# Performance work log

Hardware: AMD Instinct MI355X
Metric: run time of the kernel (lower is better)

Reference implementation:

```python
import jax, jax.numpy as jnp
import numpy as np

# Production-scale dims (see shape_source)
B, H, W, C = 8, 64, 64, 256
KH, KW = 3, 3
BASES = 16
FILTERS = 256


def setup_inputs() -> dict:
    key = jax.random.key(0)
    k1, k2, k3, k4 = jax.random.split(key, 4)
    x = jax.random.normal(k1, (B, H, W, C), dtype=jnp.float32)
    # P: channel-mixing matrix [C, C] (initialized to identity in build, then assigned)
    P = jax.random.normal(k2, (C, C), dtype=jnp.float32) * 0.05
    # Q: per-channel basis kernels [C, kh, kw, bases]
    Q = jax.random.normal(k3, (C, KH, KW, BASES), dtype=jnp.float32) * 0.1
    # S: basis-combination weights [C, bases, filters]
    S = jax.random.normal(k4, (C, BASES, FILTERS), dtype=jnp.float32) * 0.05
    return {"x": x, "P": P, "Q": Q, "S": S}


def reference(x, P, Q, S):
    # --- Step 1: channel mixing (the vectorized_map over calculate_J) ---
    # J[o] = sum_c x[..., c] * P[o, c]  ->  one GEMM over channels
    mixed = jnp.einsum('bhwc,oc->bhwo', x, P)  # [B,H,W,C]

    C_ = P.shape[0]
    kh, kw, bases = Q.shape[1], Q.shape[2], Q.shape[3]

    # --- Step 2: per-channel conv with `bases` basis kernels (the map_fn loop) ---
    # Expressed as ONE grouped (depthwise-style) conv: group c produces outputs
    # [c*bases : (c+1)*bases], matching kernel flatten order (c, b).
    rhs = jnp.transpose(Q, (1, 2, 0, 3)).reshape(kh, kw, 1, C_ * bases)  # HWIO
    dw = jax.lax.conv_general_dilated(
        mixed, rhs, window_strides=(1, 1), padding='VALID',
        dimension_numbers=('NHWC', 'HWIO', 'NHWC'),
        feature_group_count=C_,
    )  # [B, H-kh+1, W-kw+1, C*bases], channel index k = c*bases + b

    b, h, w, _ = dw.shape
    # tau in the original: [B, h, w, bases, C]
    tau = dw.reshape(b, h, w, C_, bases).transpose(0, 1, 2, 4, 3)

    # --- Step 3: basis-weighted combination (the vectorized_map over calculate_O) ---
    # Original flattens tau row-major over (bases, C) and S[:, :, f] row-major over
    # (C, bases), then does an elementwise dot over the flat axis. Replicate exactly.
    Tflat = tau.reshape(b, h, w, bases * C_)          # flat index k = b_idx*C + c
    Sflat = S.reshape(C_ * bases, S.shape[-1])        # flat index k = c*bases + b_idx
    O = jnp.einsum('bhwk,kf->bhwf', Tflat, Sflat)     # [B, h, w, filters]
    return O
```

## Files before the change

kernel.cpp:

```cpp
#include <hip/hip_runtime.h>
#include <hip/hip_bf16.h>

typedef __attribute__((ext_vector_type(4))) float f32x4;
typedef __attribute__((ext_vector_type(8))) short bf16x8;

#define M_TOT 30752

__device__ __forceinline__ unsigned short f2bf(float f) {
  unsigned int u = __float_as_uint(f);
  u = u + 0x7FFF + ((u >> 16) & 1);
  return (unsigned short)(u >> 16);
}

__device__ __forceinline__ void gload16(const void* g, void* l) {
  __builtin_amdgcn_global_load_lds((const __attribute__((address_space(1))) unsigned int*)g,
                                   (__attribute__((address_space(3))) unsigned int*)l,
                                   16, 0, 0);
}

__global__ __launch_bounds__(256) void prep1(const float* __restrict__ x,
                                             const float* __restrict__ Q,
                                             const float* __restrict__ S,
                                             unsigned short* __restrict__ xb,
                                             float* __restrict__ Keff) {
  const int bid = blockIdx.x;
  const int t = threadIdx.x;

  if (bid < 4096) {
    int i = bid * 256 + t;
    const f32x4* xp = (const f32x4*)x;
    f32x4 a = xp[2 * i];
    f32x4 b = xp[2 * i + 1];
    bf16x8 o;
    o[0] = (short)f2bf(a[0]); o[1] = (short)f2bf(a[1]);
    o[2] = (short)f2bf(a[2]); o[3] = (short)f2bf(a[3]);
    o[4] = (short)f2bf(b[0]); o[5] = (short)f2bf(b[1]);
    o[6] = (short)f2bf(b[2]); o[7] = (short)f2bf(b[3]);
    ((bf16x8*)xb)[i] = o;
    return;
  }

  const int o = bid - 4096;
  float s[16];
  const float* sp = S + (o >> 4) * 4096 + (o & 15) * 256 + t;
#pragma unroll
  for (int bi = 0; bi < 16; ++bi) s[bi] = sp[bi * 65536];
  const float* qp = Q + o * 144;
#pragma unroll
  for (int kk = 0; kk < 9; ++kk) {
    float a = 0.f;
#pragma unroll
    for (int bi = 0; bi < 16; ++bi) a = fmaf(qp[kk * 16 + bi], s[bi], a);
    Keff[(o * 9 + kk) * 256 + t] = a;
  }
}

__global__ __launch_bounds__(256) void k2t_k(const float* __restrict__ P,
                                             const float* __restrict__ Keff,
                                             unsigned short* __restrict__ K2t) {
  const int kk = blockIdx.x >> 6;
  const int f0 = (blockIdx.x & 63) * 4;
  const int ci = threadIdx.x;
  float acc[4] = {0.f, 0.f, 0.f, 0.f};
#pragma unroll 8
  for (int o = 0; o < 256; ++o) {
    float pv = P[o * 256 + ci];
    const float* ke = Keff + (o * 9 + kk) * 256 + f0;
    acc[0] = fmaf(pv, ke[0], acc[0]);
    acc[1] = fmaf(pv, ke[1], acc[1]);
    acc[2] = fmaf(pv, ke[2], acc[2]);
    acc[3] = fmaf(pv, ke[3], acc[3]);
  }
#pragma unroll
  for (int j = 0; j < 4; ++j)
    K2t[kk * 65536 + (f0 + j) * 256 + ci] = f2bf(acc[j]);
}

__global__ __launch_bounds__(256, 2) void conv_gemm(const unsigned short* __restrict__ xb,
                                                    const unsigned short* __restrict__ K2t,
                                                    float* __restrict__ out) {
  __shared__ __attribute__((aligned(16))) char smem[65536];

  const int tid = threadIdx.x;
  const int lane = tid & 63;
  const int wid = tid >> 6;
  const int sk = wid >> 1;
  const int wn = wid & 1;

  const int wgid = (blockIdx.x & 7) * 61 + (blockIdx.x >> 3);
  if (wgid >= 482) return;
  const int mt = wgid >> 1;
  const int nt = wgid & 1;
  const int m0 = mt * 128;
  const int n0 = nt * 128;

  const int rl = lane & 15;
  const int kg = lane >> 4;

  const int s_src = ((tid & 3) ^ ((tid >> 3) & 3)) * 8;
  int gA0, gA1;
  {
    int m = m0 + (tid >> 2); if (m >= M_TOT) m = M_TOT - 1;
    int b = m / 3844; int rem = m - b * 3844;
    int h = rem / 62; int w = rem - h * 62;
    gA0 = ((b * 64 + h) * 64 + w) * 256 + s_src;
    m = m0 + (tid >> 2) + 64; if (m >= M_TOT) m = M_TOT - 1;
    b = m / 3844; rem = m - b * 3844;
    h = rem / 62; w = rem - h * 62;
    gA1 = ((b * 64 + h) * 64 + w) * 256 + s_src;
  }
  const int fB0 = (n0 + (tid >> 2)) * 256 + s_src;
  const int fB1 = (n0 + (tid >> 2) + 64) * 256 + s_src;

  f32x4 zero = {0.f, 0.f, 0.f, 0.f};
  f32x4 acc[8][4];
#pragma unroll
  for (int i = 0; i < 8; ++i)
#pragma unroll
    for (int j = 0; j < 4; ++j) acc[i][j] = zero;

  const int slotr = (kg ^ ((rl >> 1) & 3)) * 16;
  const int aoff = sk * 8192 + rl * 64 + slotr;
  const int boff = 16384 + sk * 8192 + (wn * 64 + rl) * 64 + slotr;

#define STAGE(t, base)                                                         \
  {                                                                            \
    int kk_ = (t) >> 2, cb_ = (t) & 3;                                         \
    int kh_ = kk_ / 3, kw_ = kk_ - kh_ * 3;                                    \
    int offA_ = kh_ * 16384 + kw_ * 256 + cb_ * 64;                            \
    int offB_ = kk_ * 65536 + cb_ * 64;                                        \
    unsigned short* bA = (unsigned short*)(base);                              \
    unsigned short* bB = (unsigned short*)((char*)(base) + 16384);             \
    gload16(xb + gA0 + offA_,      bA + tid * 8);                              \
    gload16(xb + gA1 + offA_,      bA + (tid + 256) * 8);                      \
    gload16(xb + gA0 + offA_ + 32, bA + (tid + 512) * 8);                      \
    gload16(xb + gA1 + offA_ + 32, bA + (tid + 768) * 8);                      \
    gload16(K2t + offB_ + fB0,      bB + tid * 8);                             \
    gload16(K2t + offB_ + fB1,      bB + (tid + 256) * 8);                     \
    gload16(K2t + offB_ + fB0 + 32, bB + (tid + 512) * 8);                     \
    gload16(K2t + offB_ + fB1 + 32, bB + (tid + 768) * 8);                     \
  }

  STAGE(0, smem);

  for (int t = 0; t < 36; ++t) {
    char* cur = smem + (t & 1) * 32768;
    if (t < 35) STAGE(t + 1, smem + ((t + 1) & 1) * 32768);
    if (t == 35) asm volatile("s_waitcnt vmcnt(0)" ::: "memory");
    else         asm volatile("s_waitcnt vmcnt(8)" ::: "memory");
    __builtin_amdgcn_sched_barrier(0);
    __builtin_amdgcn_s_barrier();
    __builtin_amdgcn_sched_barrier(0);

    bf16x8 bfr[4];
#pragma unroll
    for (int ni = 0; ni < 4; ++ni)
      bfr[ni] = *(const bf16x8*)(cur + boff + ni * 1024);
    bf16x8 a0 = *(const bf16x8*)(cur + aoff);
    bf16x8 a1 = *(const bf16x8*)(cur + aoff + 1024);
#pragma unroll
    for (int j = 0; j < 4; ++j) {
      bf16x8 a2, a3;
      if (j < 3) {
        a2 = *(const bf16x8*)(cur + aoff + (2 * j + 2) * 1024);
        a3 = *(const bf16x8*)(cur + aoff + (2 * j + 3) * 1024);
      }
      __builtin_amdgcn_s_setprio(1);
#pragma unroll
      for (int ni = 0; ni < 4; ++ni)
        acc[2 * j][ni] = __builtin_amdgcn_mfma_f32_16x16x32_bf16(
            a0, bfr[ni], acc[2 * j][ni], 0, 0, 0);
#pragma unroll
      for (int ni = 0; ni < 4; ++ni)
        acc[2 * j + 1][ni] = __builtin_amdgcn_mfma_f32_16x16x32_bf16(
            a1, bfr[ni], acc[2 * j + 1][ni], 0, 0, 0);
      __builtin_amdgcn_s_setprio(0);
      a0 = a2; a1 = a3;
    }

    __builtin_amdgcn_sched_barrier(0);
    __builtin_amdgcn_s_barrier();
    __builtin_amdgcn_sched_barrier(0);
  }

  float* red = (float*)smem;
  if (sk == 1) {
#pragma unroll
    for (int mi = 0; mi < 8; ++mi)
#pragma unroll
      for (int ni = 0; ni < 4; ++ni)
        *(f32x4*)((char*)red + (((wn * 8 + mi) * 4 + ni) * 64 + lane) * 16) =
            acc[mi][ni];
  }
  __syncthreads();
  if (sk == 0) {
#pragma unroll
    for (int mi = 0; mi < 8; ++mi) {
      int mb = m0 + mi * 16 + kg * 4;
#pragma unroll
      for (int ni = 0; ni < 4; ++ni) {
        f32x4 o = *(f32x4*)((char*)red + (((wn * 8 + mi) * 4 + ni) * 64 + lane) * 16);
        o += acc[mi][ni];
        int f = n0 + wn * 64 + ni * 16 + rl;
#pragma unroll
        for (int r = 0; r < 4; ++r) {
          int m = mb + r;
          if (m < M_TOT) out[m * 256 + f] = o[r];
        }
      }
    }
  }
#undef STAGE
}

extern "C" void kernel_launch(void* const* d_in, const int* in_sizes, int n_in,
                              void* d_out, int out_size, void* d_ws, size_t ws_size,
                              hipStream_t stream) {
  const float* x = (const float*)d_in[0];
  const float* P = (const float*)d_in[1];
  const float* Q = (const float*)d_in[2];
  const float* S = (const float*)d_in[3];
  float* out = (float*)d_out;

  char* ws = (char*)d_ws;
  unsigned short* xb   = (unsigned short*)ws;
  unsigned short* K2t  = (unsigned short*)(ws + 16777216);
  float*          Keff = (float*)(ws + 16777216 + 1179648);

  prep1<<<4096 + 256, 256, 0, stream>>>(x, Q, S, xb, Keff);
  k2t_k<<<576, 256, 0, stream>>>(P, Keff, K2t);
  conv_gemm<<<488, 256, 0, stream>>>(xb, K2t, out);
}
```

Before: 76.92 us.

## Fuse fp32-to-bf16 conversion of x into conv GEMM A-tile staging

Drops the separate prep pass that converted all of x to bf16 in a workspace buffer. The GEMM now loads fp32 x straight into registers, packs it to bf16 with v_cvt_pk_bf16_f32, and writes it to LDS after the MFMA phase, while the B tile keeps using direct global-to-LDS loads. This removes a full read and write of x (and one launch) but doubles the A-tile global bytes per stage, since the same x rows are re-read across the 9 kernel taps and 2 N tiles, and it adds register pressure and changes the barrier pattern.

```diff
diff --git a/kernel.cpp b/kernel.cpp
--- a/kernel.cpp
+++ b/kernel.cpp
@@ -3,6 +3,7 @@
 
 typedef __attribute__((ext_vector_type(4))) float f32x4;
 typedef __attribute__((ext_vector_type(8))) short bf16x8;
+typedef __attribute__((ext_vector_type(4))) unsigned int u32x4;
 
 #define M_TOT 30752
 
@@ -18,29 +19,14 @@
                                    16, 0, 0);
 }
 
-__global__ __launch_bounds__(256) void prep1(const float* __restrict__ x,
-                                             const float* __restrict__ Q,
-                                             const float* __restrict__ S,
-                                             unsigned short* __restrict__ xb,
-                                             float* __restrict__ Keff) {
-  const int bid = blockIdx.x;
+#define CVT_PK(dst, lo, hi) \
+  asm("v_cvt_pk_bf16_f32 %0, %1, %2" : "=v"(dst) : "v"(lo), "v"(hi))
+
+__global__ __launch_bounds__(256) void keff_k(const float* __restrict__ Q,
+                                              const float* __restrict__ S,
+                                              float* __restrict__ Keff) {
+  const int o = blockIdx.x;
   const int t = threadIdx.x;
-
-  if (bid < 4096) {
-    int i = bid * 256 + t;
-    const f32x4* xp = (const f32x4*)x;
-    f32x4 a = xp[2 * i];
-    f32x4 b = xp[2 * i + 1];
-    bf16x8 o;
-    o[0] = (short)f2bf(a[0]); o[1] = (short)f2bf(a[1]);
-    o[2] = (short)f2bf(a[2]); o[3] = (short)f2bf(a[3]);
-    o[4] = (short)f2bf(b[0]); o[5] = (short)f2bf(b[1]);
-    o[6] = (short)f2bf(b[2]); o[7] = (short)f2bf(b[3]);
-    ((bf16x8*)xb)[i] = o;
-    return;
-  }
-
-  const int o = bid - 4096;
   float s[16];
   const float* sp = S + (o >> 4) * 4096 + (o & 15) * 256 + t;
 #pragma unroll
@@ -76,7 +62,7 @@
     K2t[kk * 65536 + (f0 + j) * 256 + ci] = f2bf(acc[j]);
 }
 
-__global__ __launch_bounds__(256, 2) void conv_gemm(const unsigned short* __restrict__ xb,
+__global__ __launch_bounds__(256, 2) void conv_gemm(const float* __restrict__ x,
                                                     const unsigned short* __restrict__ K2t,
                                                     float* __restrict__ out) {
   __shared__ __attribute__((aligned(16))) char smem[65536];
@@ -119,35 +105,71 @@
 #pragma unroll
     for (int j = 0; j < 4; ++j) acc[i][j] = zero;
 
+  f32x4 av[8];
+
   const int slotr = (kg ^ ((rl >> 1) & 3)) * 16;
   const int aoff = sk * 8192 + rl * 64 + slotr;
   const int boff = 16384 + sk * 8192 + (wn * 64 + rl) * 64 + slotr;
 
-#define STAGE(t, base)                                                         \
+#define A_LOAD(t)                                                              \
   {                                                                            \
     int kk_ = (t) >> 2, cb_ = (t) & 3;                                         \
     int kh_ = kk_ / 3, kw_ = kk_ - kh_ * 3;                                    \
     int offA_ = kh_ * 16384 + kw_ * 256 + cb_ * 64;                            \
+    const f32x4* p0 = (const f32x4*)(x + gA0 + offA_);                         \
+    const f32x4* p1 = (const f32x4*)(x + gA1 + offA_);                         \
+    av[0] = p0[0]; av[1] = p0[1];                                              \
+    av[2] = p1[0]; av[3] = p1[1];                                              \
+    av[4] = p0[8]; av[5] = p0[9];                        \
+    av[6] = p1[8]; av[7] = p1[9];                                              \
+  }
+
+#define STAGE_B(t, base)                                                       \
+  {                                                                            \
+    int kk_ = (t) >> 2, cb_ = (t) & 3;                                         \
     int offB_ = kk_ * 65536 + cb_ * 64;                                        \
-    unsigned short* bA = (unsigned short*)(base);                              \
     unsigned short* bB = (unsigned short*)((char*)(base) + 16384);             \
-    gload16(xb + gA0 + offA_,      bA + tid * 8);                              \
-    gload16(xb + gA1 + offA_,      bA + (tid + 256) * 8);                      \
-    gload16(xb + gA0 + offA_ + 32, bA + (tid + 512) * 8);                      \
-    gload16(xb + gA1 + offA_ + 32, bA + (tid + 768) * 8);                      \
     gload16(K2t + offB_ + fB0,      bB + tid * 8);                             \
     gload16(K2t + offB_ + fB1,      bB + (tid + 256) * 8);                     \
     gload16(K2t + offB_ + fB0 + 32, bB + (tid + 512) * 8);                     \
     gload16(K2t + offB_ + fB1 + 32, bB + (tid + 768) * 8);                     \
   }
 
-  STAGE(0, smem);
+#define A_WRITE(base)                                                          \
+  {                                                                            \
+    unsigned short* bA = (unsigned short*)(base);                              \
+    _Pragma("unroll")                                                          \
+    for (int q = 0; q < 4; ++q) {                                              \
+      unsigned int w0, w1, w2, w3;                                             \
+      CVT_PK(w0, av[2 * q][0], av[2 * q][1]);                                  \
+      CVT_PK(w1, av[2 * q][2], av[2 * q][3]);                                  \
+      CVT_PK(w2, av[2 * q + 1][0], av[2 * q + 1][1]);                          \
+      CVT_PK(w3, av[2 * q + 1][2], av[2 * q + 1][3]);                          \
+      u32x4 w = {w0, w1, w2, w3};                                              \
+      *(u32x4*)(bA + (tid + 256 * q) * 8) = w;              \
+    }                                                                          \
+  }
+
+  A_LOAD(0);
+  __builtin_amdgcn_sched_barrier(0);
+  STAGE_B(0, smem);
+  asm volatile("s_waitcnt vmcnt(4)" ::: "memory");
+  __builtin_amdgcn_sched_barrier(0);
+  A_WRITE(smem);
 
   for (int t = 0; t < 36; ++t) {
     char* cur = smem + (t & 1) * 32768;
-    if (t < 35) STAGE(t + 1, smem + ((t + 1) & 1) * 32768);
-    if (t == 35) asm volatile("s_waitcnt vmcnt(0)" ::: "memory");
-    else         asm volatile("s_waitcnt vmcnt(8)" ::: "memory");
+    char* nxt = smem + ((t + 1) & 1) * 32768;
+
+    if (t < 35) {
+      A_LOAD(t + 1);
+      __builtin_amdgcn_sched_barrier(0);
+      STAGE_B(t + 1, nxt);
+      asm volatile("s_waitcnt vmcnt(12)" ::: "memory");
+    } else {
+      asm volatile("s_waitcnt vmcnt(0)" ::: "memory");
+    }
+    asm volatile("s_waitcnt lgkmcnt(0)" ::: "memory");
     __builtin_amdgcn_sched_barrier(0);
     __builtin_amdgcn_s_barrier();
     __builtin_amdgcn_sched_barrier(0);
@@ -178,12 +200,15 @@
       a0 = a2; a1 = a3;
     }
 
-    __builtin_amdgcn_sched_barrier(0);
-    __builtin_amdgcn_s_barrier();
-    __builtin_amdgcn_sched_barrier(0);
+    if (t < 35) {
+      asm volatile("s_waitcnt vmcnt(4)" ::: "memory");
+      __builtin_amdgcn_sched_barrier(0);
+      A_WRITE(nxt);
+    }
   }
 
   float* red = (float*)smem;
+  __syncthreads();
   if (sk == 1) {
 #pragma unroll
     for (int mi = 0; mi < 8; ++mi)
@@ -210,7 +235,9 @@
       }
     }
   }
-#undef STAGE
+#undef A_LOAD
+#undef STAGE_B
+#undef A_WRITE
 }
 
 extern "C" void kernel_launch(void* const* d_in, const int* in_sizes, int n_in,
@@ -223,11 +250,10 @@
   float* out = (float*)d_out;
 
   char* ws = (char*)d_ws;
-  unsigned short* xb   = (unsigned short*)ws;
-  unsigned short* K2t  = (unsigned short*)(ws + 16777216);
-  float*          Keff = (float*)(ws + 16777216 + 1179648);
-
-  prep1<<<4096 + 256, 256, 0, stream>>>(x, Q, S, xb, Keff);
+  unsigned short* K2t  = (unsigned short*)ws;
+  float*          Keff = (float*)(ws + 1179648);
+
+  keff_k<<<256, 256, 0, stream>>>(Q, S, Keff);
   k2t_k<<<576, 256, 0, stream>>>(P, Keff, K2t);
-  conv_gemm<<<488, 256, 0, stream>>>(xb, K2t, out);
-}
+  conv_gemm<<<488, 256, 0, stream>>>(x, K2t, out);
+}
```

After: 83.98 us. +9.2%, slower.
